# Kernel tuning notes

Hardware: AMD Instinct MI355X
Metric: run time of the kernel (lower is better)

## Reference

```python
import jax, jax.numpy as jnp
import numpy as np

HIDDEN = 128
N_H = 32
E = 262144


def setup_inputs() -> dict:
    key = jax.random.key(0)
    ks = jax.random.split(key, 10)
    s = lambda fan_in: 1.0 / np.sqrt(fan_in)
    return {
        "h_i": jax.random.normal(ks[0], (E, N_H), dtype=jnp.float32),
        "e_ij": jax.random.normal(ks[1], (E, 1), dtype=jnp.float32),
        # lin_A1: 1 -> HIDDEN
        "W_A1": jax.random.uniform(ks[2], (1, HIDDEN), jnp.float32, -s(1), s(1)),
        "b_A1": jnp.zeros((HIDDEN,), jnp.float32),
        # lin_A2: HIDDEN -> N_H*N_H
        "W_A2": jax.random.uniform(ks[3], (HIDDEN, N_H * N_H), jnp.float32, -s(HIDDEN), s(HIDDEN)),
        "b_A2": jnp.zeros((N_H * N_H,), jnp.float32),
        # lin_b1: 1 -> HIDDEN
        "W_b1": jax.random.uniform(ks[4], (1, HIDDEN), jnp.float32, -s(1), s(1)),
        "b_b1": jnp.zeros((HIDDEN,), jnp.float32),
        # lin_b2: HIDDEN -> N_H
        "W_b2": jax.random.uniform(ks[5], (HIDDEN, N_H), jnp.float32, -s(HIDDEN), s(HIDDEN)),
        "b_b2": jnp.zeros((N_H,), jnp.float32),
    }


def reference(h_i, e_ij, W_A1, b_A1, W_A2, b_A2, W_b1, b_b1, W_b2, b_b2):
    # Per-edge MLP producing an [N_H, N_H] matrix A from the scalar edge feature
    A = jax.nn.selu(e_ij @ W_A1 + b_A1)          # [E, HIDDEN]
    A = (A @ W_A2 + b_A2).reshape(-1, N_H, N_H)  # [E, N_H, N_H]
    # Per-edge MLP producing an [N_H] bias b
    b = jax.nn.selu(e_ij @ W_b1 + b_b1)          # [E, HIDDEN]
    b = b @ W_b2 + b_b2                          # [E, N_H]
    # Batched matvec: m_ij[e, i] = sum_j A[e, i, j] * h_i[e, j] + b[e, i]
    m_ij = jnp.einsum('eij,ej->ei', A, h_i) + b
    return m_ij
```

## Files before the change

kernel.cpp:

```cpp
#include <hip/hip_runtime.h>

#define NH        32
#define HID       128
#define E_TOT     262144
#define CH_ELEM   8192
#define NCH_MAIN  16
#define TAIL_OFF  131072
#define TAIL_ELEM 8192

typedef float        f32x4 __attribute__((ext_vector_type(4)));
typedef short        s16x8 __attribute__((ext_vector_type(8)));
typedef unsigned int u32x4 __attribute__((ext_vector_type(4)));

static __device__ __forceinline__ short f2bf(float f) {
    __bf16 b = (__bf16)f;
    return __builtin_bit_cast(short, b);
}
static __device__ __forceinline__ float selu_f(float x) {
    const float kScale  = 1.0507009873554804934193349852946f;
    const float kAlphaS = 1.7580993408473768599402175208123f;
    float neg = kAlphaS * (__expf(x) - 1.0f);
    return x > 0.0f ? kScale * x : neg;
}

__global__ void wt_build(const float* __restrict__ W_A2, const float* __restrict__ b_A2,
                         const float* __restrict__ W_b2, unsigned short* __restrict__ WT) {
    int gid = blockIdx.x * 256 + threadIdx.x;
    if (gid >= TAIL_OFF + TAIL_ELEM) return;
    int it, g, lrow, p, kap;
    if (gid < TAIL_OFF) {
        int c  = gid >> 14;
        int r  = gid & 16383;
        int sl = r >> 10;
        it   = (r >> 9) & 1;
        g    = (r >> 7) & 3;
        lrow = (r >> 3) & 15;
        p    = r & 7;
        kap  = c * 512 + sl * 32 + g * 8 + p;
    } else {
        int r  = gid - TAIL_OFF;
        int sl = r >> 10;
        it   = (r >> 9) & 1;
        g    = (r >> 7) & 3;
        lrow = (r >> 3) & 15;
        p    = r & 7;
        kap  = 4096 + sl * 32 + g * 8 + p;
    }
    int i = it * 16 + lrow;
    float v = 0.0f;
    if (kap < 4096)      v = W_A2[(kap >> 5) * 1024 + i * 32 + (kap & 31)];
    else if (kap < 4128) v = b_A2[i * 32 + (kap - 4096)];
    else if (kap < 4256) v = W_b2[(kap - 4128) * 32 + i];
    WT[gid] = (unsigned short)f2bf(v);
}

typedef const __attribute__((address_space(1))) unsigned int GU32;
typedef __attribute__((address_space(3))) unsigned int LU32;
static __device__ __forceinline__ void gload_lds16(const void* g, void* l) {
    __builtin_amdgcn_global_load_lds((GU32*)g, (LU32*)l, 16, 0, 0);
}

__global__ void __launch_bounds__(256, 4)
msg_main(const float* __restrict__ h_i, const float* __restrict__ e_ij,
         const float* __restrict__ W_A1, const float* __restrict__ b_A1,
         const float* __restrict__ W_b1, const float* __restrict__ b_b1,
         const float* __restrict__ b_b2,
         const unsigned short* __restrict__ WT,
         float* __restrict__ out)
{
    __shared__ unsigned short ldsW[CH_ELEM];
    __shared__ float cA1[HID], cBA1[HID], cB1a[HID], cB1b[HID], cb2[NH];

    const int tid  = threadIdx.x;
    const int lane = tid & 63;
    const int wid  = tid >> 6;
    const int lrow = lane & 15;
    const int g    = lane >> 4;
    const int e0   = blockIdx.x * 256 + wid * 64;

    if (tid < HID) {
        cA1[tid]  = W_A1[tid];
        cBA1[tid] = b_A1[tid];
        cB1a[tid] = W_b1[tid];
        cB1b[tid] = b_b1[tid];
    }
    if (tid < NH) cb2[tid] = b_b2[tid];

    const float ev_own = e_ij[e0 + lane];

    s16x8 hb[4];
    #pragma unroll
    for (int ct = 0; ct < 4; ++ct) {
        int er = e0 + ct * 16 + lrow;
        const float* hp = h_i + er * 32 + g * 8;
        f32x4 h0 = *(const f32x4*)hp;
        f32x4 h1 = *(const f32x4*)(hp + 4);
        #pragma unroll
        for (int p = 0; p < 4; ++p) {
            hb[ct][p]     = f2bf(h0[p]);
            hb[ct][p + 4] = f2bf(h1[p]);
        }
    }

    float ev_ct[4];
    #pragma unroll
    for (int ct = 0; ct < 4; ++ct) ev_ct[ct] = __shfl(ev_own, ct * 16 + lrow);

    f32x4 acc[4][2];
    #pragma unroll
    for (int ct = 0; ct < 4; ++ct)
        #pragma unroll
        for (int it = 0; it < 2; ++it)
            acc[ct][it] = (f32x4){0.f, 0.f, 0.f, 0.f};
    const f32x4 zf = (f32x4){0.f, 0.f, 0.f, 0.f};

    float u_own[8];

    __syncthreads();

    for (int c = 0; c < NCH_MAIN; ++c) {
        #pragma unroll
        for (int r = 0; r < 4; ++r) {
            int eo = r * 2048 + tid * 8;
            gload_lds16(WT + c * CH_ELEM + eo, &ldsW[eo]);
        }
        #pragma unroll
        for (int sl = 0; sl < 8; ++sl) {
            int s = c * 8 + sl;
            u_own[sl] = selu_f(fmaf(ev_own, cA1[s], cBA1[s]));
        }
        __syncthreads();

        #pragma unroll
        for (int sl = 0; sl < 8; ++sl) {
            u32x4 r0 = *(const u32x4*)&ldsW[sl * 1024 +       lane * 8];
            u32x4 r1 = *(const u32x4*)&ldsW[sl * 1024 + 512 + lane * 8];
            s16x8 A0 = __builtin_bit_cast(s16x8, r0);
            s16x8 A1 = __builtin_bit_cast(s16x8, r1);
            f32x4 u4[4];
            #pragma unroll
            for (int ct = 0; ct < 4; ++ct) {
                float uv = __shfl(u_own[sl], ct * 16 + lrow);
                u4[ct] = (f32x4){uv, uv, uv, uv};
            }
            {
                f32x4 t[4];
                #pragma unroll
                for (int ct = 0; ct < 4; ++ct)
                    t[ct] = __builtin_amdgcn_mfma_f32_16x16x32_bf16(A0, hb[ct], zf, 0, 0, 0);
                #pragma unroll
                for (int ct = 0; ct < 4; ++ct)
                    acc[ct][0] = __builtin_elementwise_fma(t[ct], u4[ct], acc[ct][0]);
            }
            {
                f32x4 t[4];
                #pragma unroll
                for (int ct = 0; ct < 4; ++ct)
                    t[ct] = __builtin_amdgcn_mfma_f32_16x16x32_bf16(A1, hb[ct], zf, 0, 0, 0);
                #pragma unroll
                for (int ct = 0; ct < 4; ++ct)
                    acc[ct][1] = __builtin_elementwise_fma(t[ct], u4[ct], acc[ct][1]);
            }
        }
        __syncthreads();
    }

    #pragma unroll
    for (int r = 0; r < 3; ++r) {
        int eo = r * 2048 + tid * 8;
        gload_lds16(WT + TAIL_OFF + eo, &ldsW[eo]);
    }
    __syncthreads();

    {
        u32x4 r0 = *(const u32x4*)&ldsW[      lane * 8];
        u32x4 r1 = *(const u32x4*)&ldsW[512 + lane * 8];
        s16x8 A0 = __builtin_bit_cast(s16x8, r0);
        s16x8 A1 = __builtin_bit_cast(s16x8, r1);
        #pragma unroll
        for (int ct = 0; ct < 4; ++ct) {
            acc[ct][0] = __builtin_amdgcn_mfma_f32_16x16x32_bf16(A0, hb[ct], acc[ct][0], 0, 0, 0);
            acc[ct][1] = __builtin_amdgcn_mfma_f32_16x16x32_bf16(A1, hb[ct], acc[ct][1], 0, 0, 0);
        }
    }
    #pragma unroll
    for (int q = 0; q < 4; ++q) {
        u32x4 r0 = *(const u32x4*)&ldsW[(q + 1) * 1024 +       lane * 8];
        u32x4 r1 = *(const u32x4*)&ldsW[(q + 1) * 1024 + 512 + lane * 8];
        s16x8 A0 = __builtin_bit_cast(s16x8, r0);
        s16x8 A1 = __builtin_bit_cast(s16x8, r1);
        int tb = q * 32 + g * 8;
        f32x4 wb0 = *(const f32x4*)&cB1a[tb];
        f32x4 wb1 = *(const f32x4*)&cB1a[tb + 4];
        f32x4 bb0 = *(const f32x4*)&cB1b[tb];
        f32x4 bb1 = *(const f32x4*)&cB1b[tb + 4];
        #pragma unroll
        for (int ct = 0; ct < 4; ++ct) {
            s16x8 B;
            #pragma unroll
            for (int p = 0; p < 4; ++p) {
                B[p]     = f2bf(selu_f(fmaf(ev_ct[ct], wb0[p], bb0[p])));
                B[p + 4] = f2bf(selu_f(fmaf(ev_ct[ct], wb1[p], bb1[p])));
            }
            acc[ct][0] = __builtin_amdgcn_mfma_f32_16x16x32_bf16(A0, B, acc[ct][0], 0, 0, 0);
            acc[ct][1] = __builtin_amdgcn_mfma_f32_16x16x32_bf16(A1, B, acc[ct][1], 0, 0, 0);
        }
    }

    #pragma unroll
    for (int it = 0; it < 2; ++it) {
        f32x4 b2v = *(const f32x4*)&cb2[it * 16 + g * 4];
        #pragma unroll
        for (int ct = 0; ct < 4; ++ct) {
            int edge = e0 + ct * 16 + lrow;
            f32x4 vo = acc[ct][it] + b2v;
            *(f32x4*)&out[edge * 32 + it * 16 + g * 4] = vo;
        }
    }
}

extern "C" void kernel_launch(void* const* d_in, const int* in_sizes, int n_in,
                              void* d_out, int out_size, void* d_ws, size_t ws_size,
                              hipStream_t stream) {
    const float* h_i  = (const float*)d_in[0];
    const float* e_ij = (const float*)d_in[1];
    const float* W_A1 = (const float*)d_in[2];
    const float* b_A1 = (const float*)d_in[3];
    const float* W_A2 = (const float*)d_in[4];
    const float* b_A2 = (const float*)d_in[5];
    const float* W_b1 = (const float*)d_in[6];
    const float* b_b1 = (const float*)d_in[7];
    const float* W_b2 = (const float*)d_in[8];
    const float* b_b2 = (const float*)d_in[9];

    unsigned short* WT = (unsigned short*)d_ws;

    wt_build<<<(TAIL_OFF + TAIL_ELEM + 255) / 256, 256, 0, stream>>>(W_A2, b_A2, W_b2, WT);
    msg_main<<<E_TOT / 256, 256, 0, stream>>>(h_i, e_ij, W_A1, b_A1, W_b1, b_b1,
                                              b_b2, WT, (float*)d_out);
}
```

Baseline: 97.30 us.

## Read weight fragments directly from global memory instead of staging in LDS

Removes the LDS staging buffer for the transformed weight matrix and the per-chunk global-to-LDS async loads. Each wave now loads its MFMA A-fragments straight from global memory, relying on L1/L2 caching since all waves read the same data. This drops the two block-wide barriers per chunk and frees LDS, which may raise occupancy. In exchange every wave issues redundant global loads and the load latency is no longer hidden behind a barrier-synchronised staging step.

```diff
diff --git a/kernel.cpp b/kernel.cpp
--- a/kernel.cpp
+++ b/kernel.cpp
@@ -54,12 +54,6 @@
     WT[gid] = (unsigned short)f2bf(v);
 }
 
-typedef const __attribute__((address_space(1))) unsigned int GU32;
-typedef __attribute__((address_space(3))) unsigned int LU32;
-static __device__ __forceinline__ void gload_lds16(const void* g, void* l) {
-    __builtin_amdgcn_global_load_lds((GU32*)g, (LU32*)l, 16, 0, 0);
-}
-
 __global__ void __launch_bounds__(256, 4)
 msg_main(const float* __restrict__ h_i, const float* __restrict__ e_ij,
          const float* __restrict__ W_A1, const float* __restrict__ b_A1,
@@ -68,7 +62,6 @@
          const unsigned short* __restrict__ WT,
          float* __restrict__ out)
 {
-    __shared__ unsigned short ldsW[CH_ELEM];
     __shared__ float cA1[HID], cBA1[HID], cB1a[HID], cB1b[HID], cb2[NH];
 
     const int tid  = threadIdx.x;
@@ -118,23 +111,20 @@
 
     __syncthreads();
 
+    const unsigned short* wbase = WT + lane * 8;
+
     for (int c = 0; c < NCH_MAIN; ++c) {
-        #pragma unroll
-        for (int r = 0; r < 4; ++r) {
-            int eo = r * 2048 + tid * 8;
-            gload_lds16(WT + c * CH_ELEM + eo, &ldsW[eo]);
-        }
         #pragma unroll
         for (int sl = 0; sl < 8; ++sl) {
             int s = c * 8 + sl;
             u_own[sl] = selu_f(fmaf(ev_own, cA1[s], cBA1[s]));
         }
-        __syncthreads();
 
         #pragma unroll
         for (int sl = 0; sl < 8; ++sl) {
-            u32x4 r0 = *(const u32x4*)&ldsW[sl * 1024 +       lane * 8];
-            u32x4 r1 = *(const u32x4*)&ldsW[sl * 1024 + 512 + lane * 8];
+            const unsigned short* wp = wbase + c * CH_ELEM + sl * 1024;
+            u32x4 r0 = *(const u32x4*)(wp);
+            u32x4 r1 = *(const u32x4*)(wp + 512);
             s16x8 A0 = __builtin_bit_cast(s16x8, r0);
             s16x8 A1 = __builtin_bit_cast(s16x8, r1);
             f32x4 u4[4];
@@ -162,19 +152,12 @@
                     acc[ct][1] = __builtin_elementwise_fma(t[ct], u4[ct], acc[ct][1]);
             }
         }
-        __syncthreads();
-    }
-
-    #pragma unroll
-    for (int r = 0; r < 3; ++r) {
-        int eo = r * 2048 + tid * 8;
-        gload_lds16(WT + TAIL_OFF + eo, &ldsW[eo]);
-    }
-    __syncthreads();
+    }
 
     {
-        u32x4 r0 = *(const u32x4*)&ldsW[      lane * 8];
-        u32x4 r1 = *(const u32x4*)&ldsW[512 + lane * 8];
+        const unsigned short* wp = wbase + TAIL_OFF;
+        u32x4 r0 = *(const u32x4*)(wp);
+        u32x4 r1 = *(const u32x4*)(wp + 512);
         s16x8 A0 = __builtin_bit_cast(s16x8, r0);
         s16x8 A1 = __builtin_bit_cast(s16x8, r1);
         #pragma unroll
@@ -185,8 +168,9 @@
     }
     #pragma unroll
     for (int q = 0; q < 4; ++q) {
-        u32x4 r0 = *(const u32x4*)&ldsW[(q + 1) * 1024 +       lane * 8];
-        u32x4 r1 = *(const u32x4*)&ldsW[(q + 1) * 1024 + 512 + lane * 8];
+        const unsigned short* wp = wbase + TAIL_OFF + (q + 1) * 1024;
+        u32x4 r0 = *(const u32x4*)(wp);
+        u32x4 r1 = *(const u32x4*)(wp + 512);
         s16x8 A0 = __builtin_bit_cast(s16x8, r0);
         s16x8 A1 = __builtin_bit_cast(s16x8, r1);
         int tb = q * 32 + g * 8;
```

Result: no change. 98.04 us (+0.8%).
